# Performance work log

Measured on AMD Instinct MI355X. Metric: run time of the kernel, lower is better.

The kernel has to match this reference:

```python
import jax, jax.numpy as jnp
import numpy as np

NUM_CLASSES = 4      # config.class_num (malaria stages)
N = 2048             # total nodes = source + target samples
S = 1024             # source_length
FEAT_IN = 25088      # VGG19 include_top=False -> 7*7*512 flattened
D_FC = 512           # Dense(512)
D_G1 = 512           # config.features_dim (GCNConv1 out)
D_G2 = 256           # config.GCN_hidderlayer_dim_num (GCNConv2 out)


def setup_inputs() -> dict:
    key = jax.random.key(0)
    ks = jax.random.split(key, 8)
    sc = lambda fan_in: np.float32(1.0 / np.sqrt(fan_in))
    return {
        "x": jax.random.normal(ks[0], (N, FEAT_IN), jnp.float32),
        "W_fc": jax.random.normal(ks[1], (FEAT_IN, D_FC), jnp.float32) * sc(FEAT_IN),
        "b_fc": jnp.zeros((D_FC,), jnp.float32),
        "W_g1": jax.random.normal(ks[2], (D_FC, D_G1), jnp.float32) * sc(D_FC),
        "b_g1": jnp.zeros((D_G1,), jnp.float32),
        "W_g2": jax.random.normal(ks[3], (D_G1, D_G2), jnp.float32) * sc(D_G1),
        "b_g2": jnp.zeros((D_G2,), jnp.float32),
        "source_labels": jax.random.randint(ks[4], (S,), 0, NUM_CLASSES),
        "source_length": S,
    }


def reference(x, W_fc, b_fc, W_g1, b_g1, W_g2, b_g2, source_labels, source_length):
    # fc after (omitted frozen) VGG19 backbone + flatten
    feats = x @ W_fc + b_fc                                   # [N, 512]

    # get_centers: per-class SUM of source features (no averaging, faithful)
    src = feats[:source_length]                               # [S, 512]
    centers = jax.ops.segment_sum(src, source_labels, num_segments=NUM_CLASSES)  # [C, 512]

    # per-target euclidean distance to each centroid + argmin
    # (argmin of squared distance == argmin of euclidean distance)
    tgt = feats[source_length:]                               # [T, 512]
    d2 = (jnp.sum(tgt * tgt, axis=1, keepdims=True)
          - 2.0 * (tgt @ centers.T)
          + jnp.sum(centers * centers, axis=1)[None, :])      # [T, C]
    target_labels = jnp.argmin(d2, axis=1)                    # [T] int

    # label-cluster graph: edge iff same label; source block forced to identity
    all_labels = jnp.concatenate([source_labels.astype(jnp.int32),
                                  target_labels.astype(jnp.int32)])
    adj = (all_labels[:, None] == all_labels[None, :]).astype(feats.dtype)  # [N, N]
    adj = adj.at[:source_length, :source_length].set(
        jnp.eye(source_length, dtype=feats.dtype))

    # add_self_loops(value=1) then symmetric gcn_filter D^-1/2 A D^-1/2
    A = adj + jnp.eye(N, dtype=feats.dtype)
    dinv = jax.lax.rsqrt(jnp.sum(A, axis=1))                  # [N]
    A_norm = dinv[:, None] * A * dinv[None, :]                # [N, N]

    # two GCN layers (spektral GCNConv: A_norm @ (X @ W) + b) with relu
    h = jax.nn.relu(A_norm @ (feats @ W_g1) + b_g1)           # [N, 512]
    h = jax.nn.relu(A_norm @ (h @ W_g2) + b_g2)               # [N, 256]
    return (h, A_norm, feats)
```

## Files before the change

kernel.cpp:

```cpp
#include <hip/hip_runtime.h>

#define NROWS 2048
#define SLEN  1024
#define FEAT  25088
#define DFC   512
#define DG1   512
#define DG2   256
#define CSPLIT 128

typedef __attribute__((ext_vector_type(8))) short short8;
typedef __attribute__((ext_vector_type(4))) float f32x4;

__device__ __forceinline__ unsigned short bfbits(float f) {
  unsigned int u = __float_as_uint(f);
  u += 0x7fffu + ((u >> 16) & 1u);
  return (unsigned short)(u >> 16);
}

__device__ __forceinline__ void load_lds16(const void* g, void* l) {
  __builtin_amdgcn_global_load_lds(
      (const __attribute__((address_space(1))) unsigned int*)g,
      (__attribute__((address_space(3))) unsigned int*)l, 16, 0, 0);
}

__global__ void transpose_cvt_k(const float* __restrict__ src, unsigned short* __restrict__ dst,
                                int K, int Ncol) {
  __shared__ float tile[64][65];
  int kb = blockIdx.x * 64, nb = blockIdx.y * 64;
  int tx = threadIdx.x & 63, ty = threadIdx.x >> 6;
  #pragma unroll
  for (int i = ty; i < 64; i += 4)
    tile[i][tx] = src[(size_t)(kb + i) * Ncol + (nb + tx)];
  __syncthreads();
  #pragma unroll
  for (int i = ty; i < 64; i += 4)
    dst[(size_t)(nb + i) * K + (kb + tx)] = bfbits(tile[tx][i]);
}

template<bool AF32>
__global__ __launch_bounds__(256) void gemm_k(const void* __restrict__ Aptr,
    const unsigned short* __restrict__ BT, float* __restrict__ Cacc,
    int K, int Ncols, int tiles_n, int ksteps) {
  __shared__ unsigned short Al[128 * 64];
  __shared__ unsigned short Bl[128 * 64];
  int tid = threadIdx.x;
  int m0 = (blockIdx.x / tiles_n) * 128;
  int n0 = (blockIdx.x % tiles_n) * 128;
  int kbase = blockIdx.y * ksteps * 64;
  int wid = tid >> 6, lane = tid & 63;
  int wm = wid >> 1, wn = wid & 1;
  int lrow = lane & 15, lko = lane >> 4;

  f32x4 acc[4][4];
  #pragma unroll
  for (int i = 0; i < 4; i++)
    #pragma unroll
    for (int j = 0; j < 4; j++) acc[i][j] = (f32x4){0.f, 0.f, 0.f, 0.f};

  for (int t = 0; t < ksteps; ++t) {
    int k0 = kbase + t * 64;
    __syncthreads();
    if constexpr (AF32) {
      const float* A = (const float*)Aptr;
      #pragma unroll
      for (int j = 0; j < 4; j++) {
        int ch = tid + j * 256;
        int r = ch >> 3, c = ch & 7;
        const float* g = A + (size_t)(m0 + r) * K + k0 + c * 8;
        float4 v0 = *reinterpret_cast<const float4*>(g);
        float4 v1 = *reinterpret_cast<const float4*>(g + 4);
        unsigned int w0 = (unsigned)bfbits(v0.x) | ((unsigned)bfbits(v0.y) << 16);
        unsigned int w1 = (unsigned)bfbits(v0.z) | ((unsigned)bfbits(v0.w) << 16);
        unsigned int w2 = (unsigned)bfbits(v1.x) | ((unsigned)bfbits(v1.y) << 16);
        unsigned int w3 = (unsigned)bfbits(v1.z) | ((unsigned)bfbits(v1.w) << 16);
        int p = c ^ (r & 7);
        int4 o; o.x = (int)w0; o.y = (int)w1; o.z = (int)w2; o.w = (int)w3;
        *reinterpret_cast<int4*>((char*)Al + r * 128 + p * 16) = o;
      }
    } else {
      const unsigned short* A = (const unsigned short*)Aptr;
      #pragma unroll
      for (int j = 0; j < 4; j++) {
        int chb = j * 256 + wid * 64;
        int ch = chb + lane;
        int r = ch >> 3, c = (ch & 7) ^ (r & 7);
        load_lds16(A + (size_t)(m0 + r) * K + k0 + c * 8, (char*)Al + chb * 16);
      }
    }
    #pragma unroll
    for (int j = 0; j < 4; j++) {
      int chb = j * 256 + wid * 64;
      int ch = chb + lane;
      int r = ch >> 3, c = (ch & 7) ^ (r & 7);
      load_lds16(BT + (size_t)(n0 + r) * K + k0 + c * 8, (char*)Bl + chb * 16);
    }
    __syncthreads();
    #pragma unroll
    for (int kk = 0; kk < 2; kk++) {
      short8 af[4], bfv[4];
      #pragma unroll
      for (int mi = 0; mi < 4; mi++) {
        int R = wm * 64 + mi * 16 + lrow;
        int slot = ((kk << 2) | lko) ^ (lrow & 7);
        af[mi] = *reinterpret_cast<const short8*>((char*)Al + R * 128 + slot * 16);
      }
      #pragma unroll
      for (int ni = 0; ni < 4; ni++) {
        int R = wn * 64 + ni * 16 + lrow;
        int slot = ((kk << 2) | lko) ^ (lrow & 7);
        bfv[ni] = *reinterpret_cast<const short8*>((char*)Bl + R * 128 + slot * 16);
      }
      #pragma unroll
      for (int mi = 0; mi < 4; mi++)
        #pragma unroll
        for (int ni = 0; ni < 4; ni++)
          acc[mi][ni] = __builtin_amdgcn_mfma_f32_16x16x32_bf16(af[mi], bfv[ni], acc[mi][ni], 0, 0, 0);
    }
  }
  #pragma unroll
  for (int mi = 0; mi < 4; mi++)
    #pragma unroll
    for (int ni = 0; ni < 4; ni++)
      #pragma unroll
      for (int r = 0; r < 4; r++) {
        int row = m0 + wm * 64 + mi * 16 + lko * 4 + r;
        int col = n0 + wn * 64 + ni * 16 + lrow;
        atomicAdd(&Cacc[(size_t)row * Ncols + col], acc[mi][ni][r]);
      }
}

__global__ void feats_fin_k(const float* __restrict__ facc, const float* __restrict__ bfc,
                            float* __restrict__ outf, unsigned short* __restrict__ outbf) {
  int i = blockIdx.y;
  int n = blockIdx.x * 256 + threadIdx.x;
  float v = facc[(size_t)i * DFC + n] + bfc[n];
  outf[(size_t)i * DFC + n] = v;
  outbf[(size_t)i * DFC + n] = bfbits(v);
}

__global__ void seg_sum_part_k(const float* __restrict__ x, const int* __restrict__ slab,
                               float* __restrict__ sxp) {
  int k4 = blockIdx.x * 256 + threadIdx.x;
  if (k4 >= FEAT / 4) return;
  int k = k4 * 4;
  int i0 = blockIdx.y * 64, i1 = i0 + 64;
  float4 a0 = {0,0,0,0}, a1 = {0,0,0,0}, a2 = {0,0,0,0}, a3 = {0,0,0,0};
  #pragma unroll 4
  for (int i = i0; i < i1; i++) {
    float4 v = *reinterpret_cast<const float4*>(x + (size_t)i * FEAT + k);
    int c = slab[i];
    float m0 = (c == 0) ? 1.f : 0.f, m1 = (c == 1) ? 1.f : 0.f;
    float m2 = (c == 2) ? 1.f : 0.f, m3 = (c == 3) ? 1.f : 0.f;
    a0.x += m0 * v.x; a0.y += m0 * v.y; a0.z += m0 * v.z; a0.w += m0 * v.w;
    a1.x += m1 * v.x; a1.y += m1 * v.y; a1.z += m1 * v.z; a1.w += m1 * v.w;
    a2.x += m2 * v.x; a2.y += m2 * v.y; a2.z += m2 * v.z; a2.w += m2 * v.w;
    a3.x += m3 * v.x; a3.y += m3 * v.y; a3.z += m3 * v.z; a3.w += m3 * v.w;
  }
  size_t base = (size_t)blockIdx.y * 4 * FEAT;
  *reinterpret_cast<float4*>(sxp + base + 0 * FEAT + k) = a0;
  *reinterpret_cast<float4*>(sxp + base + 1 * FEAT + k) = a1;
  *reinterpret_cast<float4*>(sxp + base + 2 * FEAT + k) = a2;
  *reinterpret_cast<float4*>(sxp + base + 3 * FEAT + k) = a3;
}

__global__ void seg_sum_reduce_k(const float* __restrict__ sxp, float* __restrict__ sx) {
  int k4 = blockIdx.x * 256 + threadIdx.x;
  if (k4 >= FEAT / 4) return;
  int k = k4 * 4;
  int c = blockIdx.y;
  double s0 = 0, s1 = 0, s2 = 0, s3 = 0;
  #pragma unroll
  for (int p = 0; p < 16; p++) {
    float4 v = *reinterpret_cast<const float4*>(sxp + ((size_t)p * 4 + c) * FEAT + k);
    s0 += (double)v.x; s1 += (double)v.y; s2 += (double)v.z; s3 += (double)v.w;
  }
  float4 r; r.x = (float)s0; r.y = (float)s1; r.z = (float)s2; r.w = (float)s3;
  *reinterpret_cast<float4*>(sx + (size_t)c * FEAT + k) = r;
}

__global__ void count_src_k(const int* __restrict__ slab, int* __restrict__ cnt) {
  __shared__ int c[4];
  if (threadIdx.x < 4) c[threadIdx.x] = 0;
  __syncthreads();
  for (int i = threadIdx.x; i < SLEN; i += 256) atomicAdd(&c[slab[i]], 1);
  __syncthreads();
  if (threadIdx.x < 4) cnt[threadIdx.x] = c[threadIdx.x];
}

__global__ void centers_part_k(const float* __restrict__ sx, const float* __restrict__ W,
                               double* __restrict__ cpart) {
  int n = blockIdx.x * 64 + (threadIdx.x & 63);
  int cc = threadIdx.x >> 6;
  int kb = blockIdx.y * (FEAT / CSPLIT), ke = kb + FEAT / CSPLIT;
  const float* sr = sx + (size_t)cc * FEAT;
  double acc = 0.0;
  #pragma unroll 4
  for (int k = kb; k < ke; k++)
    acc += (double)sr[k] * (double)W[(size_t)k * DFC + n];
  cpart[((size_t)blockIdx.y * 4 + cc) * DFC + n] = acc;
}

__global__ void centers_reduce_k(const double* __restrict__ cpart, const float* __restrict__ bfc,
                                 const int* __restrict__ cntsrc, float* __restrict__ Cent) {
  int idx = blockIdx.x * 256 + threadIdx.x;
  int cc = idx >> 9, n = idx & 511;
  double s = 0.0;
  #pragma unroll 4
  for (int p = 0; p < CSPLIT; p++) s += cpart[((size_t)p * 4 + cc) * DFC + n];
  Cent[idx] = (float)(s + (double)cntsrc[cc] * (double)bfc[n]);
}

__global__ void wc_k(const float* __restrict__ W, const float* __restrict__ Cent,
                     float* __restrict__ wc) {
  __shared__ float cs[4 * DFC];
  for (int i = threadIdx.x; i < 4 * DFC; i += 256) cs[i] = Cent[i];
  __syncthreads();
  int k = blockIdx.x * 256 + threadIdx.x;
  if (k >= FEAT) return;
  const float* wr = W + (size_t)k * DFC;
  double a0 = 0, a1 = 0, a2 = 0, a3 = 0;
  #pragma unroll 2
  for (int n = 0; n < DFC; n += 4) {
    float4 w4 = *reinterpret_cast<const float4*>(wr + n);
    a0 += (double)w4.x * cs[0 * DFC + n] + (double)w4.y * cs[0 * DFC + n + 1]
        + (double)w4.z * cs[0 * DFC + n + 2] + (double)w4.w * cs[0 * DFC + n + 3];
    a1 += (double)w4.x * cs[1 * DFC + n] + (double)w4.y * cs[1 * DFC + n + 1]
        + (double)w4.z * cs[1 * DFC + n + 2] + (double)w4.w * cs[1 * DFC + n + 3];
    a2 += (double)w4.x * cs[2 * DFC + n] + (double)w4.y * cs[2 * DFC + n + 1]
        + (double)w4.z * cs[2 * DFC + n + 2] + (double)w4.w * cs[2 * DFC + n + 3];
    a3 += (double)w4.x * cs[3 * DFC + n] + (double)w4.y * cs[3 * DFC + n + 1]
        + (double)w4.z * cs[3 * DFC + n + 2] + (double)w4.w * cs[3 * DFC + n + 3];
  }
  float4 r; r.x = (float)a0; r.y = (float)a1; r.z = (float)a2; r.w = (float)a3;
  *reinterpret_cast<float4*>(wc + 4 * (size_t)k) = r;
}

__global__ void kj_k(const float* __restrict__ Cent, const float* __restrict__ bfc,
                     float* __restrict__ Kj) {
  int j = threadIdx.x >> 6, lane = threadIdx.x & 63;
  float cn = 0.f, bc = 0.f;
  for (int n = lane; n < DFC; n += 64) {
    float c = Cent[j * DFC + n];
    cn += c * c; bc += bfc[n] * c;
  }
  #pragma unroll
  for (int m = 32; m >= 1; m >>= 1) { cn += __shfl_xor(cn, m); bc += __shfl_xor(bc, m); }
  if (lane == 0) Kj[j] = cn - 2.f * bc;
}

__global__ void d2_labels_k(const float* __restrict__ x, const float* __restrict__ wc,
                            const float* __restrict__ Kj, int* __restrict__ tlab) {
  int row = blockIdx.x;
  int tid = threadIdx.x;
  const float* xr = x + (size_t)(SLEN + row) * FEAT;
  double a0 = 0, a1 = 0, a2 = 0, a3 = 0;
  #pragma unroll 2
  for (int k = tid; k < FEAT; k += 256) {
    float xv = xr[k];
    float4 w4 = *reinterpret_cast<const float4*>(wc + 4 * (size_t)k);
    a0 += (double)xv * w4.x; a1 += (double)xv * w4.y;
    a2 += (double)xv * w4.z; a3 += (double)xv * w4.w;
  }
  #pragma unroll
  for (int m = 32; m >= 1; m >>= 1) {
    a0 += __shfl_xor(a0, m); a1 += __shfl_xor(a1, m);
    a2 += __shfl_xor(a2, m); a3 += __shfl_xor(a3, m);
  }
  __shared__ double s[4][4];
  int wid = tid >> 6, lane = tid & 63;
  if (lane == 0) { s[wid][0] = a0; s[wid][1] = a1; s[wid][2] = a2; s[wid][3] = a3; }
  __syncthreads();
  if (tid == 0) {
    double t0 = s[0][0] + s[1][0] + s[2][0] + s[3][0];
    double t1 = s[0][1] + s[1][1] + s[2][1] + s[3][1];
    double t2 = s[0][2] + s[1][2] + s[2][2] + s[3][2];
    double t3 = s[0][3] + s[1][3] + s[2][3] + s[3][3];
    double s0 = (double)Kj[0] - 2.0 * t0;
    double s1 = (double)Kj[1] - 2.0 * t1;
    double s2 = (double)Kj[2] - 2.0 * t2;
    double s3 = (double)Kj[3] - 2.0 * t3;
    int bi = 0; double b = s0;
    if (s1 < b) { b = s1; bi = 1; }
    if (s2 < b) { b = s2; bi = 2; }
    if (s3 < b) { b = s3; bi = 3; }
    tlab[row] = bi;
  }
}

__global__ void finalize_labels_k(const int* __restrict__ slab, const int* __restrict__ tlab,
                                  const int* __restrict__ cntsrc, int* __restrict__ alllab,
                                  float* __restrict__ dinv) {
  __shared__ int ct[4];
  if (threadIdx.x < 4) ct[threadIdx.x] = 0;
  __syncthreads();
  for (int i = threadIdx.x; i < SLEN; i += 256) atomicAdd(&ct[tlab[i]], 1);
  __syncthreads();
  for (int i = threadIdx.x; i < NROWS; i += 256) {
    int lab = (i < SLEN) ? slab[i] : tlab[i - SLEN];
    alllab[i] = lab;
    float rs = (i < SLEN) ? (2.f + (float)ct[lab])
                          : (1.f + (float)cntsrc[lab] + (float)ct[lab]);
    dinv[i] = 1.f / sqrtf(rs);
  }
}

__global__ void anorm_k(const int* __restrict__ alllab, const float* __restrict__ dinv,
                        float* __restrict__ Aout) {
  int i = blockIdx.y;
  int j0 = (blockIdx.x * 256 + threadIdx.x) * 4;
  int li = alllab[i];
  float di = dinv[i];
  int4 lj = *reinterpret_cast<const int4*>(alllab + j0);
  float4 dj = *reinterpret_cast<const float4*>(dinv + j0);
  int jj[4] = {lj.x, lj.y, lj.z, lj.w};
  float dd[4] = {dj.x, dj.y, dj.z, dj.w};
  float4 o;
  float* op = &o.x;
  #pragma unroll
  for (int e = 0; e < 4; e++) {
    int j = j0 + e;
    float v;
    if (i == j) v = 2.f * di * dd[e];
    else if (i < SLEN && j < SLEN) v = 0.f;
    else v = (li == jj[e]) ? di * dd[e] : 0.f;
    op[e] = v;
  }
  *reinterpret_cast<float4*>(Aout + (size_t)i * NROWS + j0) = o;
}

__global__ void reduce_st_k(const float* __restrict__ Xacc, const int* __restrict__ alllab,
                            const float* __restrict__ dinv, float* __restrict__ ST, int D) {
  int n = blockIdx.x * 256 + threadIdx.x;
  int i0 = blockIdx.y * 32, i1 = i0 + 32;
  float s[4] = {0, 0, 0, 0}, tt[4] = {0, 0, 0, 0};
  for (int i = i0; i < i1; ++i) {
    float v = dinv[i] * Xacc[(size_t)i * D + n];
    int lab = alllab[i];
    bool src = i < SLEN;
    #pragma unroll
    for (int c = 0; c < 4; c++) {
      s[c]  += (src && lab == c) ? v : 0.f;
      tt[c] += (!src && lab == c) ? v : 0.f;
    }
  }
  #pragma unroll
  for (int c = 0; c < 4; c++) {
    atomicAdd(&ST[c * D + n], s[c]);
    atomicAdd(&ST[(4 + c) * D + n], tt[c]);
  }
}

__global__ void apply_prop_k(const float* __restrict__ Xacc, const float* __restrict__ ST,
                             const int* __restrict__ alllab, const float* __restrict__ dinv,
                             const float* __restrict__ bias, float* __restrict__ outf,
                             unsigned short* __restrict__ outbf, int D) {
  int i = blockIdx.y;
  int n = blockIdx.x * 256 + threadIdx.x;
  float dv = dinv[i];
  int lab = alllab[i];
  float xv = Xacc[(size_t)i * D + n];
  float z;
  if (i < SLEN) z = dv * (2.f * dv * xv + ST[(4 + lab) * D + n]);
  else          z = dv * (ST[lab * D + n] + ST[(4 + lab) * D + n] + dv * xv);
  z += bias[n];
  z = fmaxf(z, 0.f);
  if (outf)  outf[(size_t)i * D + n] = z;
  if (outbf) outbf[(size_t)i * D + n] = bfbits(z);
}

extern "C" void kernel_launch(void* const* d_in, const int* in_sizes, int n_in,
                              void* d_out, int out_size, void* d_ws, size_t ws_size,
                              hipStream_t stream) {
  const float* x    = (const float*)d_in[0];
  const float* Wfc  = (const float*)d_in[1];
  const float* bfc  = (const float*)d_in[2];
  const float* Wg1  = (const float*)d_in[3];
  const float* bg1  = (const float*)d_in[4];
  const float* Wg2  = (const float*)d_in[5];
  const float* bg2  = (const float*)d_in[6];
  const int*   slab = (const int*)d_in[7];

  float* out = (float*)d_out;
  float* out_h = out;
  float* out_A = out + 524288;
  float* out_f = out + 4718592;

  char* w = (char*)d_ws;
  unsigned short* wT   = (unsigned short*)(w);
  unsigned short* g1T  = (unsigned short*)(w + 25690112);
  unsigned short* g2T  = (unsigned short*)(w + 26214400);
  float* facc          = (float*)(w + 26476544);
  unsigned short* fbf  = (unsigned short*)(w + 30670848);
  float* x1acc         = (float*)(w + 32768000);
  unsigned short* h1bf = (unsigned short*)(w + 36962304);
  float* x2acc         = (float*)(w + 39059456);
  float* sx            = (float*)(w + 41156608);
  float* Cent          = (float*)(w + 41623552);
  float* wc            = (float*)(w + 41631744);
  float* Kj            = (float*)(w + 42033152);
  int*   tlab          = (int*)(w + 42033216);
  int*   alllab        = (int*)(w + 42037312);
  float* dinv          = (float*)(w + 42045504);
  int*   cntsrc        = (int*)(w + 42053696);
  float* ST1           = (float*)(w + 42053760);
  float* ST2           = (float*)(w + 42070144);

  float*  sxp     = (float*)(w + 32768000);
  double* cpart_d = (double*)(w + 39059456);

  hipMemsetAsync(facc,  0, (size_t)NROWS * DFC * 4, stream);
  hipMemsetAsync(ST1,   0, 8 * DG1 * 4, stream);
  hipMemsetAsync(ST2,   0, 8 * DG2 * 4, stream);

  transpose_cvt_k<<<dim3(FEAT / 64, DFC / 64), 256, 0, stream>>>(Wfc, wT, FEAT, DFC);
  transpose_cvt_k<<<dim3(DFC / 64, DG1 / 64), 256, 0, stream>>>(Wg1, g1T, DFC, DG1);
  transpose_cvt_k<<<dim3(DG1 / 64, DG2 / 64), 256, 0, stream>>>(Wg2, g2T, DG1, DG2);

  gemm_k<true><<<dim3(16 * 4, 8), 256, 0, stream>>>(x, wT, facc, FEAT, DFC, 4, 49);
  feats_fin_k<<<dim3(DFC / 256, NROWS), 256, 0, stream>>>(facc, bfc, out_f, fbf);

  seg_sum_part_k<<<dim3(25, 16), 256, 0, stream>>>(x, slab, sxp);
  seg_sum_reduce_k<<<dim3(25, 4), 256, 0, stream>>>(sxp, sx);
  count_src_k<<<1, 256, 0, stream>>>(slab, cntsrc);
  centers_part_k<<<dim3(DFC / 64, CSPLIT), 256, 0, stream>>>(sx, Wfc, cpart_d);
  centers_reduce_k<<<dim3(4 * DFC / 256), 256, 0, stream>>>(cpart_d, bfc, cntsrc, Cent);
  wc_k<<<dim3(FEAT / 256), 256, 0, stream>>>(Wfc, Cent, wc);
  kj_k<<<1, 256, 0, stream>>>(Cent, bfc, Kj);
  d2_labels_k<<<dim3(NROWS - SLEN), 256, 0, stream>>>(x, wc, Kj, tlab);
  finalize_labels_k<<<1, 256, 0, stream>>>(slab, tlab, cntsrc, alllab, dinv);

  anorm_k<<<dim3(NROWS / 1024, NROWS), 256, 0, stream>>>(alllab, dinv, out_A);

  hipMemsetAsync(x1acc, 0, (size_t)NROWS * DG1 * 4, stream);
  gemm_k<false><<<dim3(16 * 4, 4), 256, 0, stream>>>(fbf, g1T, x1acc, DFC, DG1, 4, 2);
  reduce_st_k<<<dim3(DG1 / 256, 64), 256, 0, stream>>>(x1acc, alllab, dinv, ST1, DG1);
  apply_prop_k<<<dim3(DG1 / 256, NROWS), 256, 0, stream>>>(x1acc, ST1, alllab, dinv, bg1,
                                                           nullptr, h1bf, DG1);

  hipMemsetAsync(x2acc, 0, (size_t)NROWS * DG2 * 4, stream);
  gemm_k<false><<<dim3(16 * 2, 8), 256, 0, stream>>>(h1bf, g2T, x2acc, DG1, DG2, 2, 1);
  reduce_st_k<<<dim3(DG2 / 256, 64), 256, 0, stream>>>(x2acc, alllab, dinv, ST2, DG2);
  apply_prop_k<<<dim3(DG2 / 256, NROWS), 256, 0, stream>>>(x2acc, ST2, alllab, dinv, bg2,
                                                           out_h, nullptr, DG2);

  (void)in_sizes; (void)n_in; (void)out_size; (void)ws_size;
}
```

Before: 381.5 us.

## Double-buffer GEMM LDS tiles and prefetch next K-step during MFMA compute

The GEMM kernel now uses two LDS buffers for the A and B tiles. The next K-step's global loads are issued before the MFMA compute on the current buffer, so load latency overlaps with math, and one barrier per iteration is removed. For fp32 A, the values are held in registers and converted with the hardware v_cvt_pk_bf16_f32 instruction after compute, replacing the manual rounding. This doubles LDS use to 64KB per block, which may reduce occupancy, and the prefetch registers raise register pressure.

```diff
diff --git a/kernel.cpp b/kernel.cpp
--- a/kernel.cpp
+++ b/kernel.cpp
@@ -17,6 +17,12 @@
   return (unsigned short)(u >> 16);
 }
 
+__device__ __forceinline__ unsigned int cvtpk(float lo, float hi) {
+  unsigned int r;
+  asm("v_cvt_pk_bf16_f32 %0, %1, %2" : "=v"(r) : "v"(lo), "v"(hi));
+  return r;
+}
+
 __device__ __forceinline__ void load_lds16(const void* g, void* l) {
   __builtin_amdgcn_global_load_lds(
       (const __attribute__((address_space(1))) unsigned int*)g,
@@ -41,8 +47,8 @@
 __global__ __launch_bounds__(256) void gemm_k(const void* __restrict__ Aptr,
     const unsigned short* __restrict__ BT, float* __restrict__ Cacc,
     int K, int Ncols, int tiles_n, int ksteps) {
-  __shared__ unsigned short Al[128 * 64];
-  __shared__ unsigned short Bl[128 * 64];
+  __shared__ unsigned short Al[2][128 * 64];
+  __shared__ unsigned short Bl[2][128 * 64];
   int tid = threadIdx.x;
   int m0 = (blockIdx.x / tiles_n) * 128;
   int n0 = (blockIdx.x % tiles_n) * 128;
@@ -57,44 +63,67 @@
     #pragma unroll
     for (int j = 0; j < 4; j++) acc[i][j] = (f32x4){0.f, 0.f, 0.f, 0.f};
 
-  for (int t = 0; t < ksteps; ++t) {
-    int k0 = kbase + t * 64;
-    __syncthreads();
-    if constexpr (AF32) {
-      const float* A = (const float*)Aptr;
-      #pragma unroll
-      for (int j = 0; j < 4; j++) {
-        int ch = tid + j * 256;
-        int r = ch >> 3, c = ch & 7;
-        const float* g = A + (size_t)(m0 + r) * K + k0 + c * 8;
-        float4 v0 = *reinterpret_cast<const float4*>(g);
-        float4 v1 = *reinterpret_cast<const float4*>(g + 4);
-        unsigned int w0 = (unsigned)bfbits(v0.x) | ((unsigned)bfbits(v0.y) << 16);
-        unsigned int w1 = (unsigned)bfbits(v0.z) | ((unsigned)bfbits(v0.w) << 16);
-        unsigned int w2 = (unsigned)bfbits(v1.x) | ((unsigned)bfbits(v1.y) << 16);
-        unsigned int w3 = (unsigned)bfbits(v1.z) | ((unsigned)bfbits(v1.w) << 16);
-        int p = c ^ (r & 7);
-        int4 o; o.x = (int)w0; o.y = (int)w1; o.z = (int)w2; o.w = (int)w3;
-        *reinterpret_cast<int4*>((char*)Al + r * 128 + p * 16) = o;
-      }
-    } else {
-      const unsigned short* A = (const unsigned short*)Aptr;
-      #pragma unroll
-      for (int j = 0; j < 4; j++) {
-        int chb = j * 256 + wid * 64;
-        int ch = chb + lane;
-        int r = ch >> 3, c = (ch & 7) ^ (r & 7);
-        load_lds16(A + (size_t)(m0 + r) * K + k0 + c * 8, (char*)Al + chb * 16);
-      }
-    }
+  float4 pa[8];
+
+  auto loadA_regs = [&](int k0) {
+    const float* A = (const float*)Aptr;
+    #pragma unroll
+    for (int j = 0; j < 4; j++) {
+      int ch = tid + j * 256;
+      int r = ch >> 3, c = ch & 7;
+      const float* g = A + (size_t)(m0 + r) * K + k0 + c * 8;
+      pa[2 * j]     = *reinterpret_cast<const float4*>(g);
+      pa[2 * j + 1] = *reinterpret_cast<const float4*>(g + 4);
+    }
+  };
+  auto cvtWriteA = [&](int buf) {
+    #pragma unroll
+    for (int j = 0; j < 4; j++) {
+      int ch = tid + j * 256;
+      int r = ch >> 3, c = ch & 7;
+      int p = c ^ (r & 7);
+      int4 o;
+      o.x = (int)cvtpk(pa[2 * j].x,     pa[2 * j].y);
+      o.y = (int)cvtpk(pa[2 * j].z,     pa[2 * j].w);
+      o.z = (int)cvtpk(pa[2 * j + 1].x, pa[2 * j + 1].y);
+      o.w = (int)cvtpk(pa[2 * j + 1].z, pa[2 * j + 1].w);
+      *reinterpret_cast<int4*>((char*)Al[buf] + r * 128 + p * 16) = o;
+    }
+  };
+  auto stageA_lds = [&](int buf, int k0) {
+    const unsigned short* A = (const unsigned short*)Aptr;
     #pragma unroll
     for (int j = 0; j < 4; j++) {
       int chb = j * 256 + wid * 64;
       int ch = chb + lane;
       int r = ch >> 3, c = (ch & 7) ^ (r & 7);
-      load_lds16(BT + (size_t)(n0 + r) * K + k0 + c * 8, (char*)Bl + chb * 16);
-    }
-    __syncthreads();
+      load_lds16(A + (size_t)(m0 + r) * K + k0 + c * 8, (char*)Al[buf] + chb * 16);
+    }
+  };
+  auto stageB = [&](int buf, int k0) {
+    #pragma unroll
+    for (int j = 0; j < 4; j++) {
+      int chb = j * 256 + wid * 64;
+      int ch = chb + lane;
+      int r = ch >> 3, c = (ch & 7) ^ (r & 7);
+      load_lds16(BT + (size_t)(n0 + r) * K + k0 + c * 8, (char*)Bl[buf] + chb * 16);
+    }
+  };
+
+  if constexpr (AF32) { loadA_regs(kbase); cvtWriteA(0); }
+  else                { stageA_lds(0, kbase); }
+  stageB(0, kbase);
+  __syncthreads();
+
+  int cur = 0;
+  for (int t = 0; t < ksteps; ++t) {
+    int k1 = kbase + (t + 1) * 64;
+    bool more = (t + 1 < ksteps);
+    if (more) {
+      if constexpr (AF32) loadA_regs(k1);
+      else                stageA_lds(cur ^ 1, k1);
+      stageB(cur ^ 1, k1);
+    }
     #pragma unroll
     for (int kk = 0; kk < 2; kk++) {
       short8 af[4], bfv[4];
@@ -102,13 +131,13 @@
       for (int mi = 0; mi < 4; mi++) {
         int R = wm * 64 + mi * 16 + lrow;
         int slot = ((kk << 2) | lko) ^ (lrow & 7);
-        af[mi] = *reinterpret_cast<const short8*>((char*)Al + R * 128 + slot * 16);
+        af[mi] = *reinterpret_cast<const short8*>((char*)Al[cur] + R * 128 + slot * 16);
       }
       #pragma unroll
       for (int ni = 0; ni < 4; ni++) {
         int R = wn * 64 + ni * 16 + lrow;
         int slot = ((kk << 2) | lko) ^ (lrow & 7);
-        bfv[ni] = *reinterpret_cast<const short8*>((char*)Bl + R * 128 + slot * 16);
+        bfv[ni] = *reinterpret_cast<const short8*>((char*)Bl[cur] + R * 128 + slot * 16);
       }
       #pragma unroll
       for (int mi = 0; mi < 4; mi++)
@@ -116,7 +145,11 @@
         for (int ni = 0; ni < 4; ni++)
           acc[mi][ni] = __builtin_amdgcn_mfma_f32_16x16x32_bf16(af[mi], bfv[ni], acc[mi][ni], 0, 0, 0);
     }
-  }
+    if constexpr (AF32) { if (more) cvtWriteA(cur ^ 1); }
+    __syncthreads();
+    cur ^= 1;
+  }
+
   #pragma unroll
   for (int mi = 0; mi < 4; mi++)
     #pragma unroll
```

Result: faster. 373.8 us (-2.0%).
